# Optimization experiments

Measured on AMD Instinct MI355X. Metric: run time of the kernel, lower is better.

## Reference

```python
import jax, jax.numpy as jnp
import numpy as np
import math

B, S, D = 16, 577, 768          # batch, seq (24*24 grid + 1 cls), in_dim=att_dim
H, HD = 12, 64                  # heads, head_dim
GRID = 24                       # height = width; S = GRID*GRID + rpe_skip
RATIO = 1.9
ALPHA, BETA, GAMMA = 1.0 * RATIO, 2.0 * RATIO, 8.0 * RATIO
BETA_INT = int(BETA)            # 3
NUM_BUCKETS = (2 * BETA_INT + 1) ** 2 + 1  # 49 product buckets + 1 extra for skip (cls) = 50


def _piecewise_index(d):
    # iRPE piecewise bucket index (numpy, static). d: integer offsets.
    d = d.astype(np.float64)
    ad = np.abs(d)
    log_part = ALPHA + np.log(np.maximum(ad, 1e-9) / ALPHA) / math.log(GAMMA / ALPHA) * (BETA - ALPHA)
    y_out = np.sign(d) * np.clip(np.round(log_part), None, BETA)
    idx = np.where(ad <= ALPHA, np.round(d), y_out)
    return np.trunc(idx).astype(np.int64)  # torch .to(int) truncates toward zero


def make_rp_bucket():
    # 2D 'product' method bucket ids with skip=1 (cls token -> extra bucket)
    ii, jj = np.meshgrid(np.arange(GRID), np.arange(GRID), indexing='ij')
    pos = np.stack([ii.ravel(), jj.ravel()], axis=-1)          # (L,2)
    diff = pos[:, None, :] - pos[None, :, :]                    # (L,L,2)
    Sb = 2 * BETA_INT + 1
    r = _piecewise_index(diff[..., 0]) + BETA_INT               # [0, 2*beta_int]
    c = _piecewise_index(diff[..., 1]) + BETA_INT
    pid = r * Sb + c                                            # [0, 48]
    L = GRID * GRID
    bucket = np.full((L + 1, L + 1), NUM_BUCKETS - 1, dtype=np.int32)
    bucket[1:, 1:] = pid
    return jnp.asarray(bucket)


def setup_inputs() -> dict:
    key = jax.random.key(0)
    k1, k2, k3 = jax.random.split(key, 3)
    x = jax.random.normal(k1, (B, S, D), dtype=jnp.float32)
    w_qkv = jax.random.normal(k2, (3 * D, D), dtype=jnp.float32) * 0.02   # torch Linear weight (out,in)
    rpe_table = jax.random.normal(k3, (HD, NUM_BUCKETS), dtype=jnp.float32) * 0.02  # shared-head contextual table
    rp_bucket = make_rp_bucket()                                # (S,S) int32
    return {"x": x, "w_qkv": w_qkv, "rpe_table": rpe_table, "rp_bucket": rp_bucket}


def reference(x, w_qkv, rpe_table, rp_bucket):
    qkv = x @ w_qkv.T                                           # (B,S,3D)
    q, k, v = jnp.split(qkv, 3, axis=-1)
    # Faithful to torch source: plain reshape (B,S,D)->(B,H,S,HD) (no transpose-split)
    scale = 1.0 / jnp.sqrt(jnp.asarray(HD, x.dtype))
    q = q.reshape(B, H, S, HD) * scale
    k = k.reshape(B, H, S, HD)
    v = v.reshape(B, H, S, HD)
    qk = jnp.einsum('bhid,bhjd->bhij', q, k)                    # (B,H,S,S)
    # contextual rpe_k: bias[b,h,i,j] = (q[b,h,i] . rpe_table[:, rp_bucket[i,j]])
    ctx = jnp.einsum('bhid,dc->bhic', q, rpe_table)             # (B,H,S,NUM_BUCKETS)
    idx = jnp.broadcast_to(rp_bucket[None, None].astype(jnp.int32), (B, H, S, S))
    bias = jnp.take_along_axis(ctx, idx, axis=-1)               # (B,H,S,S)
    att = jax.nn.softmax(qk + bias, axis=-1)
    out = jnp.einsum('bhij,bhjd->bhid', att, v)                 # (B,H,S,HD)
    y = out.transpose(0, 2, 1, 3).reshape(B, S, D)              # out_proj is Identity (out_dim==att_dim)
    return y
```

## Files before the change

### kernel.cpp

```cpp
#include <hip/hip_runtime.h>

constexpr int BN_  = 16;
constexpr int SN_  = 577;
constexpr int SP_  = 640;
constexpr int DN_  = 768;
constexpr int HN_  = 12;
constexpr int HD_  = 64;
constexpr int NB_  = 50;
constexpr int MR_  = BN_ * SN_;
constexpr int MRP_ = 73 * 128;
constexpr int NQ_  = 3 * DN_;
constexpr int BHS_ = BN_ * HN_ * SN_;
constexpr int SHD_ = SN_ * HD_;

typedef __attribute__((ext_vector_type(8))) short short8;
typedef __attribute__((ext_vector_type(4))) float f32x4;

__device__ __forceinline__ short f2bf(float f) {
  union { float f; unsigned u; } v; v.f = f;
  unsigned r = (v.u + 0x7fffu + ((v.u >> 16) & 1u)) >> 16;
  return (short)r;
}

__device__ __forceinline__ float ex2(float x) {
  float r; asm("v_exp_f32 %0, %1" : "=v"(r) : "v"(x)); return r;
}

__device__ __forceinline__ unsigned cvtpk(float a, float b) {
  unsigned r; asm("v_cvt_pk_bf16_f32 %0, %1, %2" : "=v"(r) : "v"(a), "v"(b));
  return r;
}

__device__ __forceinline__ float bf2f(unsigned short u) {
  union { unsigned u; float f; } v; v.u = ((unsigned)u) << 16; return v.f;
}

__launch_bounds__(256)
__global__ void cvt_k(const float* __restrict__ src, short* __restrict__ dst,
                      int n_src, int n_dst) {
  const int i = (blockIdx.x * 256 + threadIdx.x) * 8;
  if (i >= n_dst) return;
  union { short8 v; short u[8]; } pk;
  if (i < n_src) {
    const float4 a = *(const float4*)(src + i);
    const float4 b = *(const float4*)(src + i + 4);
    pk.u[0] = f2bf(a.x); pk.u[1] = f2bf(a.y); pk.u[2] = f2bf(a.z); pk.u[3] = f2bf(a.w);
    pk.u[4] = f2bf(b.x); pk.u[5] = f2bf(b.y); pk.u[6] = f2bf(b.z); pk.u[7] = f2bf(b.w);
  } else {
#pragma unroll
    for (int j = 0; j < 8; ++j) pk.u[j] = 0;
  }
  *(short8*)(dst + i) = pk.v;
}

__launch_bounds__(256)
__global__ void rpb8_k(const int* __restrict__ rpb, unsigned char* __restrict__ rpbu8) {
  const int tid = blockIdx.x * 256 + threadIdx.x;
  if (tid >= SN_ * 160) return;
  const int i = tid / 160, c4 = tid - i * 160;
  const int j = c4 * 4;
  uchar4 o;
  o.x = (j     < SN_) ? (unsigned char)rpb[i * SN_ + j    ] : 0;
  o.y = (j + 1 < SN_) ? (unsigned char)rpb[i * SN_ + j + 1] : 0;
  o.z = (j + 2 < SN_) ? (unsigned char)rpb[i * SN_ + j + 2] : 0;
  o.w = (j + 3 < SN_) ? (unsigned char)rpb[i * SN_ + j + 3] : 0;
  *(uchar4*)(rpbu8 + (size_t)i * 640 + j) = o;
}

__launch_bounds__(256)
__global__ void qkv_mfma_k(const short* __restrict__ xb, const short* __restrict__ wb,
                           short* __restrict__ Qbf, short* __restrict__ Ksw,
                           short* __restrict__ Vbf) {
  __shared__ short At[128 * 64];
  __shared__ short Bt[128 * 64];
  const int t = threadIdx.x;
  const int w = t >> 6, lane = t & 63, g = lane >> 4, ln = lane & 15;
  const int wm = w >> 1, wn = w & 1;
  const int m0 = blockIdx.y * 128, n0 = blockIdx.x * 128;

  const int sr = t >> 1, su = (t & 1) * 4;
  const short* ga = xb + (size_t)(m0 + sr) * DN_ + su * 8;
  const short* gb = wb + (size_t)(n0 + sr) * DN_ + su * 8;
  short* la = At + sr * 64;
  short* lb = Bt + sr * 64;
  const int swr = sr & 7;

  f32x4 acc[4][4];
#pragma unroll
  for (int mt = 0; mt < 4; ++mt)
#pragma unroll
    for (int nt = 0; nt < 4; ++nt) acc[mt][nt] = (f32x4){0.f, 0.f, 0.f, 0.f};

  short8 ra[4], rb[4];
#pragma unroll
  for (int u = 0; u < 4; ++u) {
    ra[u] = *(const short8*)(ga + u * 8);
    rb[u] = *(const short8*)(gb + u * 8);
  }

  for (int k0 = 0; k0 < DN_; k0 += 64) {
    __syncthreads();
#pragma unroll
    for (int u = 0; u < 4; ++u) {
      *(short8*)(la + (((su + u) ^ swr) * 8)) = ra[u];
      *(short8*)(lb + (((su + u) ^ swr) * 8)) = rb[u];
    }
    __syncthreads();
    if (k0 + 64 < DN_) {
#pragma unroll
      for (int u = 0; u < 4; ++u) {
        ra[u] = *(const short8*)(ga + k0 + 64 + u * 8);
        rb[u] = *(const short8*)(gb + k0 + 64 + u * 8);
      }
    }
#pragma unroll
    for (int kc = 0; kc < 2; ++kc) {
      short8 af[4], bf[4];
#pragma unroll
      for (int mt = 0; mt < 4; ++mt) {
        const int row = wm * 64 + mt * 16 + ln;
        const int u = (kc * 4 + g) ^ (row & 7);
        af[mt] = *(const short8*)&At[row * 64 + u * 8];
      }
#pragma unroll
      for (int nt = 0; nt < 4; ++nt) {
        const int row = wn * 64 + nt * 16 + ln;
        const int u = (kc * 4 + g) ^ (row & 7);
        bf[nt] = *(const short8*)&Bt[row * 64 + u * 8];
      }
#pragma unroll
      for (int mt = 0; mt < 4; ++mt)
#pragma unroll
        for (int nt = 0; nt < 4; ++nt)
          acc[mt][nt] = __builtin_amdgcn_mfma_f32_16x16x32_bf16(af[mt], bf[nt], acc[mt][nt], 0, 0, 0);
    }
  }

  const int nw0  = n0 + wn * 64;
  const int secg = nw0 / DN_;
  const int cbw  = nw0 - secg * DN_;
  const float QSC = 0.18033688011112042f;
#pragma unroll
  for (int mt = 0; mt < 4; ++mt) {
#pragma unroll
    for (int r = 0; r < 4; ++r) {
      const int gm = m0 + wm * 64 + mt * 16 + 4 * g + r;
      if (gm >= MR_) continue;
      const int bb = gm / SN_;
      const int ss = gm - bb * SN_;
      const int pb = ss * DN_ + cbw;
#pragma unroll
      for (int nt = 0; nt < 4; ++nt) {
        const int p   = pb + nt * 16 + ln;
        const int hh  = p / SHD_;
        const int rem = p - hh * SHD_;
        const int ii  = rem >> 6;
        const int dd  = rem & 63;
        const size_t ro = (size_t)(bb * HN_ + hh);
        const float v = acc[mt][nt][r];
        if (secg == 0) {
          Qbf[(ro * SN_ + ii) * 64 + dd] = f2bf(v * QSC);
        } else if (secg == 1) {
          Ksw[(ro * SP_ + ii) * 64 + (dd ^ ((ii & 7) << 3))] = f2bf(v);
        } else {
          Vbf[(ro * SP_ + ii) * 64 + dd] = f2bf(v);
        }
      }
    }
  }
}

__launch_bounds__(256)
__global__ void vtr_k(const short* __restrict__ Vbf, short* __restrict__ Vtsw) {
  __shared__ short T[64][72];
  const int t = threadIdx.x;
  const int jt = blockIdx.x, bh = blockIdx.y;
  const int j0 = jt * 64;
  {
    const int r = t >> 2, c0 = (t & 3) * 16;
    const short* src = Vbf + ((size_t)bh * SP_ + j0 + r) * 64 + c0;
    *(short8*)&T[r][c0]     = *(const short8*)(src);
    *(short8*)&T[r][c0 + 8] = *(const short8*)(src + 8);
  }
  __syncthreads();
  const int d = t >> 2;
  short* dst = Vtsw + ((size_t)bh * 64 + d) * SP_;
  const int sw = (d & 7) << 3;
#pragma unroll
  for (int e = 0; e < 4; ++e) {
    const int jl = (t & 3) * 16 + e * 4;
    const int jg = j0 + jl;
    short4 v;
    v.x = (jg + 0 < SN_) ? T[jl + 0][d] : (short)0;
    v.y = (jg + 1 < SN_) ? T[jl + 1][d] : (short)0;
    v.z = (jg + 2 < SN_) ? T[jl + 2][d] : (short)0;
    v.w = (jg + 3 < SN_) ? T[jl + 3][d] : (short)0;
    *(short4*)&dst[jg ^ sw] = v;
  }
}

__launch_bounds__(256)
__global__ void attn_k(const short* __restrict__ Qbf, const short* __restrict__ Ksw,
                       const short* __restrict__ Vtsw, const float* __restrict__ rpe,
                       const unsigned char* __restrict__ rpbu8, float* __restrict__ y) {
  __shared__ short Kt[64 * 64];
  __shared__ short Vt[64 * 64];
  __shared__ unsigned short ctxs[4][16][53];
  __shared__ char urp[8192];
  short (*Rp)[64] = (short (*)[64])urp;
  unsigned char* rpbt = (unsigned char*)urp;

  const int t = threadIdx.x;
  const int w = t >> 6, lane = t & 63, g = lane >> 4, ln = lane & 15;
  const int wg = blockIdx.x;
  const int xcd = wg & 7, idx = wg >> 3;
  const int qt = idx % 10;
  const int bh = (idx / 10) * 8 + xcd;
  const int b = bh / HN_, h = bh - b * HN_;
  const int i0 = qt * 64;
  const size_t rb = (size_t)bh * SN_;
  const short* Kbh = Ksw + (size_t)bh * SP_ * 64;
  const short* Vbh = Vtsw + (size_t)bh * 64 * SP_;

  const int sr_ = t >> 2, scu_ = (t & 3) * 16;
  const int irow_s = (i0 + sr_ <= SN_ - 1) ? (i0 + sr_) : (SN_ - 1);

  short8 kr0, kr1, vr0, vr1; int4 rp_;
  {
    const short* ks = Kbh + (size_t)sr_ * 64 + scu_;
    kr0 = *(const short8*)(ks); kr1 = *(const short8*)(ks + 8);
    const short* vs = Vbh + (size_t)sr_ * SP_ + scu_;
    vr0 = *(const short8*)(vs); vr1 = *(const short8*)(vs + 8);
    rp_ = *(const int4*)(rpbu8 + (size_t)irow_s * 640 + scu_);
  }

  for (int e = t; e < 64 * 64; e += 256) {
    const int c = e >> 6, d = e & 63;
    Rp[c][d] = (c < NB_) ? f2bf(rpe[d * NB_ + c]) : (short)0;
  }

  short8 qf[2];
  {
    int row = i0 + 16 * w + ln; if (row > SN_ - 1) row = SN_ - 1;
    const short* qp = Qbf + (rb + row) * 64;
    qf[0] = *(const short8*)(qp + 8 * g);
    qf[1] = *(const short8*)(qp + 32 + 8 * g);
  }

  __syncthreads();

  {
    f32x4 accC[4];
#pragma unroll
    for (int ct = 0; ct < 4; ++ct) accC[ct] = (f32x4){0.f, 0.f, 0.f, 0.f};
#pragma unroll
    for (int kc = 0; kc < 2; ++kc) {
#pragma unroll
      for (int ct = 0; ct < 4; ++ct) {
        const short8 rf = *(const short8*)&Rp[ct * 16 + ln][kc * 32 + 8 * g];
        accC[ct] = __builtin_amdgcn_mfma_f32_16x16x32_bf16(qf[kc], rf, accC[ct], 0, 0, 0);
      }
    }
#pragma unroll
    for (int ct = 0; ct < 4; ++ct) {
      const int c = ct * 16 + ln;
      if (c < 53) {
#pragma unroll
        for (int r = 0; r < 4; ++r)
          ctxs[w][4 * g + r][c] = (unsigned short)f2bf(accC[ct][r]);
      }
    }
  }

  float m = -3e38f, l = 0.f;
  f32x4 accO[4];
#pragma unroll
  for (int dt = 0; dt < 4; ++dt) accO[dt] = (f32x4){0.f, 0.f, 0.f, 0.f};

  const int swv = (ln & 7) << 3;
  const unsigned short* cbase = &ctxs[w][ln][0];
  const int rpoff = (16 * w + ln) * 80;

  for (int jt = 0; jt < 10; ++jt) {
    const int j0 = jt * 64;
    __syncthreads();
    *(short8*)&Kt[sr_ * 64 + scu_]     = kr0;
    *(short8*)&Kt[sr_ * 64 + scu_ + 8] = kr1;
    *(short8*)&Vt[sr_ * 64 + scu_]     = vr0;
    *(short8*)&Vt[sr_ * 64 + scu_ + 8] = vr1;
    *(int4*)&rpbt[sr_ * 80 + scu_]     = rp_;
    __syncthreads();

    if (jt < 9) {
      const int jn = j0 + 64;
      const short* ks = Kbh + (size_t)(jn + sr_) * 64 + scu_;
      kr0 = *(const short8*)(ks); kr1 = *(const short8*)(ks + 8);
      const short* vs = Vbh + (size_t)sr_ * SP_ + jn + scu_;
      vr0 = *(const short8*)(vs); vr1 = *(const short8*)(vs + 8);
      rp_ = *(const int4*)(rpbu8 + (size_t)irow_s * 640 + jn + scu_);
    }

    f32x4 accS[4];
#pragma unroll
    for (int nt = 0; nt < 4; ++nt) accS[nt] = (f32x4){0.f, 0.f, 0.f, 0.f};
    __builtin_amdgcn_s_setprio(1);
#pragma unroll
    for (int kc = 0; kc < 2; ++kc) {
      const int cb = (kc * 32 + 8 * g) ^ swv;
#pragma unroll
      for (int nt = 0; nt < 4; ++nt) {
        const short8 kf = *(const short8*)&Kt[(nt * 16 + ln) * 64 + cb];
        accS[nt] = __builtin_amdgcn_mfma_f32_16x16x32_bf16(kf, qf[kc], accS[nt], 0, 0, 0);
      }
    }
    __builtin_amdgcn_s_setprio(0);

    float pv[4][4];
#pragma unroll
    for (int nt = 0; nt < 4; ++nt) {
      const uchar4 bk = *(const uchar4*)&rpbt[rpoff + nt * 16 + 4 * g];
      pv[nt][0] = accS[nt][0] + bf2f(cbase[bk.x]);
      pv[nt][1] = accS[nt][1] + bf2f(cbase[bk.y]);
      pv[nt][2] = accS[nt][2] + bf2f(cbase[bk.z]);
      pv[nt][3] = accS[nt][3] + bf2f(cbase[bk.w]);
    }
    if (jt == 9) {
#pragma unroll
      for (int nt = 0; nt < 4; ++nt) {
        const int jb = j0 + nt * 16 + 4 * g;
#pragma unroll
        for (int r = 0; r < 4; ++r)
          if (jb + r >= SN_) pv[nt][r] = -3e38f;
      }
    }

    float mx = fmaxf(fmaxf(pv[0][0], pv[0][1]), fmaxf(pv[0][2], pv[0][3]));
#pragma unroll
    for (int nt = 1; nt < 4; ++nt)
      mx = fmaxf(mx, fmaxf(fmaxf(pv[nt][0], pv[nt][1]), fmaxf(pv[nt][2], pv[nt][3])));
    mx = fmaxf(mx, __shfl_xor(mx, 16));
    mx = fmaxf(mx, __shfl_xor(mx, 32));

    if (__any(mx > m + 8.f)) {
      const float mnew = fmaxf(m, mx);
      const float sc = ex2(m - mnew);
      float scr[4];
#pragma unroll
      for (int r = 0; r < 4; ++r) scr[r] = __shfl(sc, 4 * g + r);
#pragma unroll
      for (int dt = 0; dt < 4; ++dt)
#pragma unroll
        for (int r = 0; r < 4; ++r) accO[dt][r] *= scr[r];
      l *= sc;
      m = mnew;
    }

    float sum = 0.f;
#pragma unroll
    for (int nt = 0; nt < 4; ++nt)
#pragma unroll
      for (int r = 0; r < 4; ++r) {
        const float p = ex2(pv[nt][r] - m);
        pv[nt][r] = p;
        sum += p;
      }
    sum += __shfl_xor(sum, 16);
    sum += __shfl_xor(sum, 32);
    l += sum;

    short8 pf[2];
#pragma unroll
    for (int kc = 0; kc < 2; ++kc) {
      union { short8 v; unsigned wd[4]; } pk;
      pk.wd[0] = cvtpk(pv[2 * kc][0],     pv[2 * kc][1]);
      pk.wd[1] = cvtpk(pv[2 * kc][2],     pv[2 * kc][3]);
      pk.wd[2] = cvtpk(pv[2 * kc + 1][0], pv[2 * kc + 1][1]);
      pk.wd[3] = cvtpk(pv[2 * kc + 1][2], pv[2 * kc + 1][3]);
      pf[kc] = pk.v;
    }

    __builtin_amdgcn_s_setprio(1);
#pragma unroll
    for (int kc = 0; kc < 2; ++kc) {
#pragma unroll
      for (int dt = 0; dt < 4; ++dt) {
        const short* vrow = &Vt[(dt * 16 + ln) * 64];
        union { short8 v; short4 hh[2]; } u;
        u.hh[0] = *(const short4*)&vrow[(kc * 32 + 4 * g) ^ swv];
        u.hh[1] = *(const short4*)&vrow[(kc * 32 + 16 + 4 * g) ^ swv];
        accO[dt] = __builtin_amdgcn_mfma_f32_16x16x32_bf16(pf[kc], u.v, accO[dt], 0, 0, 0);
      }
    }
    __builtin_amdgcn_s_setprio(0);
  }

  float linv[4];
#pragma unroll
  for (int r = 0; r < 4; ++r) linv[r] = 1.f / __shfl(l, 4 * g + r);
#pragma unroll
  for (int r = 0; r < 4; ++r) {
    const int i = i0 + 16 * w + 4 * g + r;
    if (i >= SN_) continue;
    float* yp = y + ((size_t)b * SN_ + i) * DN_ + h * HD_ + ln;
#pragma unroll
    for (int dt = 0; dt < 4; ++dt) yp[dt * 16] = accO[dt][r] * linv[r];
  }
}

extern "C" void kernel_launch(void* const* d_in, const int* in_sizes, int n_in,
                              void* d_out, int out_size, void* d_ws, size_t ws_size,
                              hipStream_t stream) {
  const float* x   = (const float*)d_in[0];
  const float* w   = (const float*)d_in[1];
  const float* rpe = (const float*)d_in[2];
  const int*   rpb = (const int*)d_in[3];
  float* y = (float*)d_out;

  short* xb   = (short*)d_ws;
  short* wb   = xb + (size_t)MRP_ * DN_;
  short* Qbf  = wb + (size_t)NQ_ * DN_;
  short* Ksw  = Qbf + (size_t)BHS_ * HD_;
  short* Vbf  = Ksw + (size_t)BN_ * HN_ * SP_ * 64;
  short* Vtsw = Vbf + (size_t)BN_ * HN_ * SP_ * 64;
  unsigned char* rpbu8 = (unsigned char*)(Vtsw + (size_t)BN_ * HN_ * 64 * SP_);

  cvt_k<<<dim3(MRP_ * DN_ / 2048), 256, 0, stream>>>(x, xb, MR_ * DN_, MRP_ * DN_);
  cvt_k<<<dim3(NQ_ * DN_ / 2048), 256, 0, stream>>>(w, wb, NQ_ * DN_, NQ_ * DN_);
  rpb8_k<<<dim3((SN_ * 160 + 255) / 256), 256, 0, stream>>>(rpb, rpbu8);
  qkv_mfma_k<<<dim3(18, 73), 256, 0, stream>>>(xb, wb, Qbf, Ksw, Vbf);
  vtr_k<<<dim3(10, BN_ * HN_), 256, 0, stream>>>(Vbf, Vtsw);
  attn_k<<<dim3(1920), 256, 0, stream>>>(Qbf, Ksw, Vtsw, rpe, rpbu8, y);
}
```

Baseline: 159.4 us.

## Double-buffer K/V/bucket tiles in LDS with one barrier per iteration

Converts the attention kernel's single-buffered K, V and bucket-id LDS tiles into ping-pong buffers. Each iteration writes the next tile into the alternate buffer, prefetches the tile after that from global memory, then computes on the current buffer, so the loop needs one barrier instead of two. Global load addressing moves to a contiguous per-thread layout, and the max and sum reductions are rebalanced into trees. LDS use roughly doubles, which may lower occupancy, and the Rp table now aliases the bucket buffer, which requires an extra barrier before the first tile is stored.

```diff
diff --git a/kernel.cpp b/kernel.cpp
--- a/kernel.cpp
+++ b/kernel.cpp
@@ -203,12 +203,11 @@
 __global__ void attn_k(const short* __restrict__ Qbf, const short* __restrict__ Ksw,
                        const short* __restrict__ Vtsw, const float* __restrict__ rpe,
                        const unsigned char* __restrict__ rpbu8, float* __restrict__ y) {
-  __shared__ short Kt[64 * 64];
-  __shared__ short Vt[64 * 64];
+  __shared__ short Kt[2 * 4096];
+  __shared__ short Vt[2 * 4096];
+  __shared__ unsigned char rpbt[2 * 5120];
   __shared__ unsigned short ctxs[4][16][53];
-  __shared__ char urp[8192];
-  short (*Rp)[64] = (short (*)[64])urp;
-  unsigned char* rpbt = (unsigned char*)urp;
+  short (*Rp)[64] = (short (*)[64])rpbt;
 
   const int t = threadIdx.x;
   const int w = t >> 6, lane = t & 63, g = lane >> 4, ln = lane & 15;
@@ -222,17 +221,17 @@
   const short* Kbh = Ksw + (size_t)bh * SP_ * 64;
   const short* Vbh = Vtsw + (size_t)bh * 64 * SP_;
 
-  const int sr_ = t >> 2, scu_ = (t & 3) * 16;
-  const int irow_s = (i0 + sr_ <= SN_ - 1) ? (i0 + sr_) : (SN_ - 1);
+  const int tK = t * 8;
+  const int vRow = t >> 3, vCol = (t & 7) * 8;
+  const int rpRow = t >> 2, rpCol = (t & 3) * 16;
+  const int irow_s = (i0 + rpRow <= SN_ - 1) ? (i0 + rpRow) : (SN_ - 1);
 
   short8 kr0, kr1, vr0, vr1; int4 rp_;
-  {
-    const short* ks = Kbh + (size_t)sr_ * 64 + scu_;
-    kr0 = *(const short8*)(ks); kr1 = *(const short8*)(ks + 8);
-    const short* vs = Vbh + (size_t)sr_ * SP_ + scu_;
-    vr0 = *(const short8*)(vs); vr1 = *(const short8*)(vs + 8);
-    rp_ = *(const int4*)(rpbu8 + (size_t)irow_s * 640 + scu_);
-  }
+  kr0 = *(const short8*)(Kbh + tK);
+  kr1 = *(const short8*)(Kbh + 2048 + tK);
+  vr0 = *(const short8*)(Vbh + (size_t)vRow * SP_ + vCol);
+  vr1 = *(const short8*)(Vbh + (size_t)(32 + vRow) * SP_ + vCol);
+  rp_ = *(const int4*)(rpbu8 + (size_t)irow_s * 640 + rpCol);
 
   for (int e = t; e < 64 * 64; e += 256) {
     const int c = e >> 6, d = e & 63;
@@ -261,6 +260,7 @@
         accC[ct] = __builtin_amdgcn_mfma_f32_16x16x32_bf16(qf[kc], rf, accC[ct], 0, 0, 0);
       }
     }
+    __syncthreads();
 #pragma unroll
     for (int ct = 0; ct < 4; ++ct) {
       const int c = ct * 16 + ln;
@@ -272,6 +272,18 @@
     }
   }
 
+  *(short8*)&Kt[tK]        = kr0;
+  *(short8*)&Kt[2048 + tK] = kr1;
+  *(short8*)&Vt[tK]        = vr0;
+  *(short8*)&Vt[2048 + tK] = vr1;
+  *(int4*)&rpbt[rpRow * 80 + rpCol] = rp_;
+  kr0 = *(const short8*)(Kbh + 4096 + tK);
+  kr1 = *(const short8*)(Kbh + 4096 + 2048 + tK);
+  vr0 = *(const short8*)(Vbh + (size_t)vRow * SP_ + 64 + vCol);
+  vr1 = *(const short8*)(Vbh + (size_t)(32 + vRow) * SP_ + 64 + vCol);
+  rp_ = *(const int4*)(rpbu8 + (size_t)irow_s * 640 + 64 + rpCol);
+  __syncthreads();
+
   float m = -3e38f, l = 0.f;
   f32x4 accO[4];
 #pragma unroll
@@ -281,24 +293,28 @@
   const unsigned short* cbase = &ctxs[w][ln][0];
   const int rpoff = (16 * w + ln) * 80;
 
+  int cur = 0;
   for (int jt = 0; jt < 10; ++jt) {
-    const int j0 = jt * 64;
-    __syncthreads();
-    *(short8*)&Kt[sr_ * 64 + scu_]     = kr0;
-    *(short8*)&Kt[sr_ * 64 + scu_ + 8] = kr1;
-    *(short8*)&Vt[sr_ * 64 + scu_]     = vr0;
-    *(short8*)&Vt[sr_ * 64 + scu_ + 8] = vr1;
-    *(int4*)&rpbt[sr_ * 80 + scu_]     = rp_;
-    __syncthreads();
-
+    const int cw = cur ^ 1;
     if (jt < 9) {
-      const int jn = j0 + 64;
-      const short* ks = Kbh + (size_t)(jn + sr_) * 64 + scu_;
-      kr0 = *(const short8*)(ks); kr1 = *(const short8*)(ks + 8);
-      const short* vs = Vbh + (size_t)sr_ * SP_ + jn + scu_;
-      vr0 = *(const short8*)(vs); vr1 = *(const short8*)(vs + 8);
-      rp_ = *(const int4*)(rpbu8 + (size_t)irow_s * 640 + jn + scu_);
-    }
+      *(short8*)&Kt[cw * 4096 + tK]        = kr0;
+      *(short8*)&Kt[cw * 4096 + 2048 + tK] = kr1;
+      *(short8*)&Vt[cw * 4096 + tK]        = vr0;
+      *(short8*)&Vt[cw * 4096 + 2048 + tK] = vr1;
+      *(int4*)&rpbt[cw * 5120 + rpRow * 80 + rpCol] = rp_;
+    }
+    if (jt < 8) {
+      const int jn = jt * 64 + 128;
+      kr0 = *(const short8*)(Kbh + (size_t)jn * 64 + tK);
+      kr1 = *(const short8*)(Kbh + (size_t)jn * 64 + 2048 + tK);
+      vr0 = *(const short8*)(Vbh + (size_t)vRow * SP_ + jn + vCol);
+      vr1 = *(const short8*)(Vbh + (size_t)(32 + vRow) * SP_ + jn + vCol);
+      rp_ = *(const int4*)(rpbu8 + (size_t)irow_s * 640 + jn + rpCol);
+    }
+
+    const short* KtC = Kt + cur * 4096;
+    const short* VtC = Vt + cur * 4096;
+    const unsigned char* rpC = rpbt + cur * 5120;
 
     f32x4 accS[4];
 #pragma unroll
@@ -309,7 +325,7 @@
       const int cb = (kc * 32 + 8 * g) ^ swv;
 #pragma unroll
       for (int nt = 0; nt < 4; ++nt) {
-        const short8 kf = *(const short8*)&Kt[(nt * 16 + ln) * 64 + cb];
+        const short8 kf = *(const short8*)&KtC[(nt * 16 + ln) * 64 + cb];
         accS[nt] = __builtin_amdgcn_mfma_f32_16x16x32_bf16(kf, qf[kc], accS[nt], 0, 0, 0);
       }
     }
@@ -318,7 +334,7 @@
     float pv[4][4];
 #pragma unroll
     for (int nt = 0; nt < 4; ++nt) {
-      const uchar4 bk = *(const uchar4*)&rpbt[rpoff + nt * 16 + 4 * g];
+      const uchar4 bk = *(const uchar4*)&rpC[rpoff + nt * 16 + 4 * g];
       pv[nt][0] = accS[nt][0] + bf2f(cbase[bk.x]);
       pv[nt][1] = accS[nt][1] + bf2f(cbase[bk.y]);
       pv[nt][2] = accS[nt][2] + bf2f(cbase[bk.z]);
@@ -327,17 +343,18 @@
     if (jt == 9) {
 #pragma unroll
       for (int nt = 0; nt < 4; ++nt) {
-        const int jb = j0 + nt * 16 + 4 * g;
+        const int jb = jt * 64 + nt * 16 + 4 * g;
 #pragma unroll
         for (int r = 0; r < 4; ++r)
           if (jb + r >= SN_) pv[nt][r] = -3e38f;
       }
     }
 
-    float mx = fmaxf(fmaxf(pv[0][0], pv[0][1]), fmaxf(pv[0][2], pv[0][3]));
-#pragma unroll
-    for (int nt = 1; nt < 4; ++nt)
-      mx = fmaxf(mx, fmaxf(fmaxf(pv[nt][0], pv[nt][1]), fmaxf(pv[nt][2], pv[nt][3])));
+    float mq[4];
+#pragma unroll
+    for (int nt = 0; nt < 4; ++nt)
+      mq[nt] = fmaxf(fmaxf(pv[nt][0], pv[nt][1]), fmaxf(pv[nt][2], pv[nt][3]));
+    float mx = fmaxf(fmaxf(mq[0], mq[1]), fmaxf(mq[2], mq[3]));
     mx = fmaxf(mx, __shfl_xor(mx, 16));
     mx = fmaxf(mx, __shfl_xor(mx, 32));
 
@@ -355,15 +372,16 @@
       m = mnew;
     }
 
-    float sum = 0.f;
 #pragma unroll
     for (int nt = 0; nt < 4; ++nt)
 #pragma unroll
-      for (int r = 0; r < 4; ++r) {
-        const float p = ex2(pv[nt][r] - m);
-        pv[nt][r] = p;
-        sum += p;
-      }
+      for (int r = 0; r < 4; ++r)
+        pv[nt][r] = ex2(pv[nt][r] - m);
+    float sq[4];
+#pragma unroll
+    for (int nt = 0; nt < 4; ++nt)
+      sq[nt] = (pv[nt][0] + pv[nt][1]) + (pv[nt][2] + pv[nt][3]);
+    float sum = (sq[0] + sq[1]) + (sq[2] + sq[3]);
     sum += __shfl_xor(sum, 16);
     sum += __shfl_xor(sum, 32);
     l += sum;
@@ -384,7 +402,7 @@
     for (int kc = 0; kc < 2; ++kc) {
 #pragma unroll
       for (int dt = 0; dt < 4; ++dt) {
-        const short* vrow = &Vt[(dt * 16 + ln) * 64];
+        const short* vrow = &VtC[(dt * 16 + ln) * 64];
         union { short8 v; short4 hh[2]; } u;
         u.hh[0] = *(const short4*)&vrow[(kc * 32 + 4 * g) ^ swv];
         u.hh[1] = *(const short4*)&vrow[(kc * 32 + 16 + 4 * g) ^ swv];
@@ -392,6 +410,9 @@
       }
     }
     __builtin_amdgcn_s_setprio(0);
+
+    __syncthreads();
+    cur ^= 1;
   }
 
   float linv[4];
```

After: 162.6 us. Within noise of the previous version (+1.9%).
